# Kernel optimization log

Hardware: AMD Instinct MI355X
Metric: run time of the kernel (lower is better)

Reference implementation:

```python
import jax, jax.numpy as jnp
import numpy as np

INDIM = 1024
OUTDIM = 2048
BATCH = 8192


def _kaiming_uniform(key, shape):
    # torch kaiming_uniform_ default: a=sqrt(5) -> gain=sqrt(2/(1+5))=sqrt(1/3),
    # fan_in = shape[0] (first dim for 2D), bound = gain*sqrt(3/fan_in) = 1/sqrt(fan_in)
    fan_in = shape[0]
    bound = 1.0 / np.sqrt(fan_in)
    return jax.random.uniform(key, shape, dtype=jnp.float32, minval=-bound, maxval=bound)


def setup_inputs() -> dict:
    key = jax.random.key(0)
    kx, kp = jax.random.split(key)
    x = jax.random.normal(kx, (BATCH, INDIM), dtype=jnp.float32)
    prototypes = _kaiming_uniform(kp, (INDIM, OUTDIM))
    return {"x": x, "prototypes": prototypes}


def reference(x, prototypes):
    # score[b, o] = -sum_i (x[b,i] - P[i,o])^2
    #             = -(||x_b||^2 - 2 x_b . P_:,o + ||P_:,o||^2)
    x_sq = jnp.sum(x * x, axis=1, keepdims=True)          # [B, 1]
    p_sq = jnp.sum(prototypes * prototypes, axis=0)       # [O]
    cross = jnp.matmul(x, prototypes)                      # [B, O] GEMM
    return 2.0 * cross - x_sq - p_sq[None, :]
```

## Files before the change

kernel.cpp:

```cpp
#include <hip/hip_runtime.h>
#include <hip/hip_bf16.h>
#include <cstdint>

#define BATCH  8192
#define INDIM  1024
#define OUTDIM 2048

typedef float  f32x4   __attribute__((ext_vector_type(4)));
typedef float  f32x16  __attribute__((ext_vector_type(16)));
typedef int    i32x2   __attribute__((ext_vector_type(2)));
typedef int    i32x4   __attribute__((ext_vector_type(4)));
typedef int    i32x8   __attribute__((ext_vector_type(8)));

__device__ __forceinline__ uint32_t pk_fp8x4(float a, float b, float c, float d) {
    uint32_t v = 0;
    v = __builtin_amdgcn_cvt_pk_fp8_f32(a, b, v, false);
    v = __builtin_amdgcn_cvt_pk_fp8_f32(c, d, v, true);
    return v;
}

__device__ __forceinline__ void async_copy16(const void* g, void* l) {
    __builtin_amdgcn_global_load_lds(
        (__attribute__((address_space(1))) void*)(g),
        (__attribute__((address_space(3))) void*)(l),
        16, 0, 0);
}

__device__ __forceinline__ int k4(int r) { return (r ^ (r >> 2)) & 3; }

__global__ __launch_bounds__(256) void prep_fused(const float* __restrict__ x,
                                                  const float* __restrict__ P,
                                                  uint8_t* __restrict__ xq8,
                                                  float* __restrict__ xsq,
                                                  uint8_t* __restrict__ pt8,
                                                  float* __restrict__ psq_part) {
    __shared__ float tile[64][33];
    __shared__ float psums[32];
    const int tid = threadIdx.x;

    if (blockIdx.x < BATCH / 4) {
        const int wave = tid >> 6;
        const int lane = tid & 63;
        const int row  = blockIdx.x * 4 + wave;
        const f32x4* src = (const f32x4*)(x + (size_t)row * INDIM);
        uint32_t* dst = (uint32_t*)(xq8 + (size_t)row * INDIM);
        float s = 0.f;
#pragma unroll
        for (int w = 0; w < 4; ++w) {
            const f32x4 v = src[lane + w * 64];
            s += v.x * v.x + v.y * v.y + v.z * v.z + v.w * v.w;
            dst[lane + w * 64] = pk_fp8x4(v.x, v.y, v.z, v.w);
        }
#pragma unroll
        for (int off = 32; off > 0; off >>= 1) s += __shfl_down(s, off);
        if (lane == 0) xsq[row] = s;
        return;
    }

    const int bx   = blockIdx.x - BATCH / 4;
    const int o0   = (bx & 63) * 32;
    const int kblk = bx >> 6;
    const int k0   = kblk * 256;
    const int kk   = tid >> 3;
    const int oq   = tid & 7;
    const int so   = tid >> 3;
    const int skc  = (tid & 7) * 8;
    float a4[4] = {0.f, 0.f, 0.f, 0.f};
    if (tid < 32) psums[tid] = 0.f;
    for (int st = 0; st < 4; ++st) {
        __syncthreads();
#pragma unroll
        for (int r2 = 0; r2 < 2; ++r2) {
            const int k = r2 * 32 + kk;
            const float4 v = *(const float4*)(P + (size_t)(k0 + st * 64 + k) * OUTDIM + o0 + oq * 4);
            tile[k][oq * 4 + 0] = v.x;
            tile[k][oq * 4 + 1] = v.y;
            tile[k][oq * 4 + 2] = v.z;
            tile[k][oq * 4 + 3] = v.w;
            a4[0] += v.x * v.x; a4[1] += v.y * v.y;
            a4[2] += v.z * v.z; a4[3] += v.w * v.w;
        }
        __syncthreads();
        i32x2 w;
        w.x = pk_fp8x4(tile[skc + 0][so] * 32.f, tile[skc + 1][so] * 32.f,
                       tile[skc + 2][so] * 32.f, tile[skc + 3][so] * 32.f);
        w.y = pk_fp8x4(tile[skc + 4][so] * 32.f, tile[skc + 5][so] * 32.f,
                       tile[skc + 6][so] * 32.f, tile[skc + 7][so] * 32.f);
        *(i32x2*)(pt8 + (size_t)(o0 + so) * INDIM + k0 + st * 64 + skc) = w;
    }
#pragma unroll
    for (int e = 0; e < 4; ++e) atomicAdd(&psums[oq * 4 + e], a4[e]);
    __syncthreads();
    if (tid < 32) psq_part[(size_t)kblk * OUTDIM + o0 + tid] = psums[tid];
}

#define TM 256
#define TN 256
#define BKB 64

__global__ __launch_bounds__(512, 2) void gemm_ep(const uint8_t* __restrict__ xq8,
                                                  const uint8_t* __restrict__ pt8,
                                                  const float* __restrict__ xsq,
                                                  const float* __restrict__ psq_part,
                                                  float* __restrict__ out) {
    __shared__ __align__(16) uint8_t As[2][TM * BKB];

    const int tid  = threadIdx.x;
    const int nb   = blockIdx.x & 7;
    const int mb   = blockIdx.x >> 3;
    const int m0   = mb * TM;
    const int n0   = nb * TN;
    const int wave = tid >> 6;
    const int lane = tid & 63;
    const int wm   = (wave >> 2) * 128;
    const int wn   = (wave & 3) * 64;
    const int l31  = lane & 31;
    const int half = lane >> 5;

    const int sr0 = tid >> 2;
    const int sq0 = (tid & 3) ^ k4(sr0);
    const int sr1 = sr0 + 128;
    const int sq1 = (tid & 3) ^ k4(sr1);

    const uint8_t* bp0 = pt8 + (size_t)(n0 + wn + l31) * INDIM + half * 32;
    const uint8_t* bp1 = pt8 + (size_t)(n0 + wn + 32 + l31) * INDIM + half * 32;

    f32x16 acc[4][2];
#pragma unroll
    for (int i = 0; i < 4; ++i)
#pragma unroll
        for (int j = 0; j < 2; ++j)
#pragma unroll
            for (int e = 0; e < 16; ++e) acc[i][j][e] = 0.f;

    async_copy16(xq8 + (size_t)(m0 + sr0) * INDIM + sq0 * 16, &As[0][tid * 16]);
    async_copy16(xq8 + (size_t)(m0 + sr1) * INDIM + sq1 * 16, &As[0][(512 + tid) * 16]);
    i32x8 bv[2];
    {
        const i32x4 l0 = *(const i32x4*)(bp0);
        const i32x4 h0 = *(const i32x4*)(bp0 + 16);
        bv[0] = __builtin_shufflevector(l0, h0, 0, 1, 2, 3, 4, 5, 6, 7);
        const i32x4 l1 = *(const i32x4*)(bp1);
        const i32x4 h1 = *(const i32x4*)(bp1 + 16);
        bv[1] = __builtin_shufflevector(l1, h1, 0, 1, 2, 3, 4, 5, 6, 7);
    }
    __syncthreads();

    int cur = 0;
    for (int kb = 0; kb < INDIM; kb += BKB) {
        const bool more = (kb + BKB < INDIM);
        i32x8 bvn[2];
        if (more) {
            const int nxt = cur ^ 1;
            const int kn  = kb + BKB;
            async_copy16(xq8 + (size_t)(m0 + sr0) * INDIM + kn + sq0 * 16, &As[nxt][tid * 16]);
            async_copy16(xq8 + (size_t)(m0 + sr1) * INDIM + kn + sq1 * 16, &As[nxt][(512 + tid) * 16]);
            const i32x4 l0 = *(const i32x4*)(bp0 + kn);
            const i32x4 h0 = *(const i32x4*)(bp0 + kn + 16);
            bvn[0] = __builtin_shufflevector(l0, h0, 0, 1, 2, 3, 4, 5, 6, 7);
            const i32x4 l1 = *(const i32x4*)(bp1 + kn);
            const i32x4 h1 = *(const i32x4*)(bp1 + kn + 16);
            bvn[1] = __builtin_shufflevector(l1, h1, 0, 1, 2, 3, 4, 5, 6, 7);
        }

        i32x8 av[4];
#pragma unroll
        for (int i = 0; i < 4; ++i) {
            const int r = wm + i * 32 + l31;
            const uint8_t* base = &As[cur][r * BKB];
            const i32x4 lo = *(const i32x4*)(base + (((half << 1) | 0) ^ k4(r)) * 16);
            const i32x4 hi = *(const i32x4*)(base + (((half << 1) | 1) ^ k4(r)) * 16);
            av[i] = __builtin_shufflevector(lo, hi, 0, 1, 2, 3, 4, 5, 6, 7);
        }
#pragma unroll
        for (int i = 0; i < 4; ++i)
#pragma unroll
            for (int j = 0; j < 2; ++j)
                acc[i][j] = __builtin_amdgcn_mfma_scale_f32_32x32x64_f8f6f4(
                    av[i], bv[j], acc[i][j],
                    0 , 0 ,
                    0, 0x7F7F7F7F ,
                    0, 0x7F7F7F7F );

        __syncthreads();
        if (more) { bv[0] = bvn[0]; bv[1] = bvn[1]; }
        cur ^= 1;
    }

    const float* xsq_w = xsq + m0 + wm;
    float ps[2];
#pragma unroll
    for (int j = 0; j < 2; ++j) {
        const int n = n0 + wn + j * 32 + l31;
        ps[j] = psq_part[n] + psq_part[OUTDIM + n] +
                psq_part[2 * OUTDIM + n] + psq_part[3 * OUTDIM + n];
    }
#pragma unroll
    for (int i = 0; i < 4; ++i) {
#pragma unroll
        for (int rg = 0; rg < 16; ++rg) {
            const int rloc = (rg & 3) + 8 * (rg >> 2) + 4 * half;
            const float xs = xsq_w[i * 32 + rloc];
            float* orow = out + (size_t)(m0 + wm + i * 32 + rloc) * OUTDIM + n0 + wn + l31;
#pragma unroll
            for (int j = 0; j < 2; ++j)
                orow[j * 32] = 0.0625f * acc[i][j][rg] - xs - ps[j];
        }
    }
}

__global__ void fallback_kernel(const float* __restrict__ x,
                                const float* __restrict__ P,
                                float* __restrict__ out) {
    const int o = blockIdx.x * blockDim.x + threadIdx.x;
    const int b = blockIdx.y;
    float cr = 0.f, xq = 0.f, pq = 0.f;
    for (int i = 0; i < INDIM; ++i) {
        const float xv = x[(size_t)b * INDIM + i];
        const float pv = P[(size_t)i * OUTDIM + o];
        cr += xv * pv; xq += xv * xv; pq += pv * pv;
    }
    out[(size_t)b * OUTDIM + o] = 2.f * cr - xq - pq;
}

extern "C" void kernel_launch(void* const* d_in, const int* in_sizes, int n_in,
                              void* d_out, int out_size, void* d_ws, size_t ws_size,
                              hipStream_t stream) {
    (void)in_sizes; (void)n_in; (void)out_size;
    const float* x = (const float*)d_in[0];
    const float* P = (const float*)d_in[1];
    float* out = (float*)d_out;

    const size_t xq_bytes  = (size_t)BATCH * INDIM;
    const size_t pt_bytes  = (size_t)OUTDIM * INDIM;
    const size_t xsq_bytes = (size_t)BATCH * 4;
    const size_t psq_bytes = (size_t)4 * OUTDIM * 4;
    const size_t need = xq_bytes + pt_bytes + xsq_bytes + psq_bytes;

    if (ws_size < need) {
        fallback_kernel<<<dim3(OUTDIM / 256, BATCH), 256, 0, stream>>>(x, P, out);
        return;
    }

    uint8_t* xq8      = (uint8_t*)d_ws;
    uint8_t* pt8      = (uint8_t*)d_ws + xq_bytes;
    float*   xsq      = (float*)((char*)d_ws + xq_bytes + pt_bytes);
    float*   psq_part = xsq + BATCH;

    prep_fused<<<BATCH / 4 + (OUTDIM / 32) * (INDIM / 256), 256, 0, stream>>>(
        x, P, xq8, xsq, pt8, psq_part);
    gemm_ep<<<(BATCH / TM) * (OUTDIM / TN), 512, 0, stream>>>(xq8, pt8, xsq, psq_part, out);
}
```

Measured before the change: 128.6 us.

## Stage B operand through LDS and double the K tile to 128

Loads the prototype (B) tile into shared memory with async global-to-LDS copies, instead of each wave reading it directly from global memory into registers. Doubles the K block to 128 bytes and widens the XOR swizzle to 8 chunks. Each iteration now runs two MFMA sub-steps, halving the number of barriers. Shared memory per block grows to 128KB, which likely limits residency to one block per CU.

```diff
diff --git a/kernel.cpp b/kernel.cpp
--- a/kernel.cpp
+++ b/kernel.cpp
@@ -26,7 +26,7 @@
         16, 0, 0);
 }
 
-__device__ __forceinline__ int k4(int r) { return (r ^ (r >> 2)) & 3; }
+__device__ __forceinline__ int k8(int r) { return (r ^ (r >> 3)) & 7; }
 
 __global__ __launch_bounds__(256) void prep_fused(const float* __restrict__ x,
                                                   const float* __restrict__ P,
@@ -96,7 +96,7 @@
 
 #define TM 256
 #define TN 256
-#define BKB 64
+#define BKB 128
 
 __global__ __launch_bounds__(512, 2) void gemm_ep(const uint8_t* __restrict__ xq8,
                                                   const uint8_t* __restrict__ pt8,
@@ -104,6 +104,7 @@
                                                   const float* __restrict__ psq_part,
                                                   float* __restrict__ out) {
     __shared__ __align__(16) uint8_t As[2][TM * BKB];
+    __shared__ __align__(16) uint8_t Bs[2][TN * BKB];
 
     const int tid  = threadIdx.x;
     const int nb   = blockIdx.x & 7;
@@ -117,13 +118,12 @@
     const int l31  = lane & 31;
     const int half = lane >> 5;
 
-    const int sr0 = tid >> 2;
-    const int sq0 = (tid & 3) ^ k4(sr0);
-    const int sr1 = sr0 + 128;
-    const int sq1 = (tid & 3) ^ k4(sr1);
-
-    const uint8_t* bp0 = pt8 + (size_t)(n0 + wn + l31) * INDIM + half * 32;
-    const uint8_t* bp1 = pt8 + (size_t)(n0 + wn + 32 + l31) * INDIM + half * 32;
+    int srow[4], scg[4];
+#pragma unroll
+    for (int s = 0; s < 4; ++s) {
+        srow[s] = s * 64 + (tid >> 3);
+        scg[s]  = (tid & 7) ^ k8(srow[s]);
+    }
 
     f32x16 acc[4][2];
 #pragma unroll
@@ -133,57 +133,61 @@
 #pragma unroll
             for (int e = 0; e < 16; ++e) acc[i][j][e] = 0.f;
 
-    async_copy16(xq8 + (size_t)(m0 + sr0) * INDIM + sq0 * 16, &As[0][tid * 16]);
-    async_copy16(xq8 + (size_t)(m0 + sr1) * INDIM + sq1 * 16, &As[0][(512 + tid) * 16]);
-    i32x8 bv[2];
-    {
-        const i32x4 l0 = *(const i32x4*)(bp0);
-        const i32x4 h0 = *(const i32x4*)(bp0 + 16);
-        bv[0] = __builtin_shufflevector(l0, h0, 0, 1, 2, 3, 4, 5, 6, 7);
-        const i32x4 l1 = *(const i32x4*)(bp1);
-        const i32x4 h1 = *(const i32x4*)(bp1 + 16);
-        bv[1] = __builtin_shufflevector(l1, h1, 0, 1, 2, 3, 4, 5, 6, 7);
+#pragma unroll
+    for (int s = 0; s < 4; ++s) {
+        async_copy16(xq8 + (size_t)(m0 + srow[s]) * INDIM + scg[s] * 16,
+                     &As[0][(s * 512 + tid) * 16]);
+        async_copy16(pt8 + (size_t)(n0 + srow[s]) * INDIM + scg[s] * 16,
+                     &Bs[0][(s * 512 + tid) * 16]);
     }
     __syncthreads();
 
     int cur = 0;
     for (int kb = 0; kb < INDIM; kb += BKB) {
-        const bool more = (kb + BKB < INDIM);
-        i32x8 bvn[2];
-        if (more) {
+        if (kb + BKB < INDIM) {
             const int nxt = cur ^ 1;
             const int kn  = kb + BKB;
-            async_copy16(xq8 + (size_t)(m0 + sr0) * INDIM + kn + sq0 * 16, &As[nxt][tid * 16]);
-            async_copy16(xq8 + (size_t)(m0 + sr1) * INDIM + kn + sq1 * 16, &As[nxt][(512 + tid) * 16]);
-            const i32x4 l0 = *(const i32x4*)(bp0 + kn);
-            const i32x4 h0 = *(const i32x4*)(bp0 + kn + 16);
-            bvn[0] = __builtin_shufflevector(l0, h0, 0, 1, 2, 3, 4, 5, 6, 7);
-            const i32x4 l1 = *(const i32x4*)(bp1 + kn);
-            const i32x4 h1 = *(const i32x4*)(bp1 + kn + 16);
-            bvn[1] = __builtin_shufflevector(l1, h1, 0, 1, 2, 3, 4, 5, 6, 7);
-        }
-
-        i32x8 av[4];
-#pragma unroll
-        for (int i = 0; i < 4; ++i) {
-            const int r = wm + i * 32 + l31;
-            const uint8_t* base = &As[cur][r * BKB];
-            const i32x4 lo = *(const i32x4*)(base + (((half << 1) | 0) ^ k4(r)) * 16);
-            const i32x4 hi = *(const i32x4*)(base + (((half << 1) | 1) ^ k4(r)) * 16);
-            av[i] = __builtin_shufflevector(lo, hi, 0, 1, 2, 3, 4, 5, 6, 7);
-        }
-#pragma unroll
-        for (int i = 0; i < 4; ++i)
-#pragma unroll
-            for (int j = 0; j < 2; ++j)
-                acc[i][j] = __builtin_amdgcn_mfma_scale_f32_32x32x64_f8f6f4(
-                    av[i], bv[j], acc[i][j],
-                    0 , 0 ,
-                    0, 0x7F7F7F7F ,
-                    0, 0x7F7F7F7F );
+#pragma unroll
+            for (int s = 0; s < 4; ++s) {
+                async_copy16(xq8 + (size_t)(m0 + srow[s]) * INDIM + kn + scg[s] * 16,
+                             &As[nxt][(s * 512 + tid) * 16]);
+                async_copy16(pt8 + (size_t)(n0 + srow[s]) * INDIM + kn + scg[s] * 16,
+                             &Bs[nxt][(s * 512 + tid) * 16]);
+            }
+        }
+
+#pragma unroll
+        for (int ks = 0; ks < 2; ++ks) {
+            const int cbase = ks * 4 + half * 2;
+            i32x8 av[4], bv[2];
+#pragma unroll
+            for (int i = 0; i < 4; ++i) {
+                const int r = wm + i * 32 + l31;
+                const uint8_t* base = &As[cur][r * BKB];
+                const i32x4 lo = *(const i32x4*)(base + ((cbase + 0) ^ k8(r)) * 16);
+                const i32x4 hi = *(const i32x4*)(base + ((cbase + 1) ^ k8(r)) * 16);
+                av[i] = __builtin_shufflevector(lo, hi, 0, 1, 2, 3, 4, 5, 6, 7);
+            }
+#pragma unroll
+            for (int j = 0; j < 2; ++j) {
+                const int r = wn + j * 32 + l31;
+                const uint8_t* base = &Bs[cur][r * BKB];
+                const i32x4 lo = *(const i32x4*)(base + ((cbase + 0) ^ k8(r)) * 16);
+                const i32x4 hi = *(const i32x4*)(base + ((cbase + 1) ^ k8(r)) * 16);
+                bv[j] = __builtin_shufflevector(lo, hi, 0, 1, 2, 3, 4, 5, 6, 7);
+            }
+#pragma unroll
+            for (int i = 0; i < 4; ++i)
+#pragma unroll
+                for (int j = 0; j < 2; ++j)
+                    acc[i][j] = __builtin_amdgcn_mfma_scale_f32_32x32x64_f8f6f4(
+                        av[i], bv[j], acc[i][j],
+                        0 , 0 ,
+                        0, 0x7F7F7F7F ,
+                        0, 0x7F7F7F7F );
+        }
 
         __syncthreads();
-        if (more) { bv[0] = bvn[0]; bv[1] = bvn[1]; }
         cur ^= 1;
     }
 
```

New measurement: 116.0 us. 1.11x faster.
